# Performance work log

Hardware: AMD Instinct MI355X
Metric: run time of the kernel (lower is better)

The kernel has to match this reference:

```python
import jax, jax.numpy as jnp
import numpy as np

B, T, C = 32, 1536, 768
G, Vg = 2, 160  # num_groups, vars_per_group (num_vars=320)
TEMP = 2.0


def setup_inputs() -> dict:
    key = jax.random.key(0)
    kx, kg, kw, kc = jax.random.split(key, 4)
    x = jax.random.normal(kx, (B, T, C), dtype=jnp.float32)
    # Gumbel(0,1) noise, equivalent to torch's -log(Exp(1).sample())
    gumbel = jax.random.gumbel(kg, (B, T, G, Vg), dtype=jnp.float32)
    W_proj = jax.random.normal(kw, (C, G * Vg), dtype=jnp.float32) * (1.0 / np.sqrt(C))
    b_proj = jnp.zeros((G * Vg,), dtype=jnp.float32)
    codebook = jax.random.normal(kc, (G, Vg, C), dtype=jnp.float32)
    return {"x": x, "gumbel": gumbel, "W_proj": W_proj, "b_proj": b_proj, "codebook": codebook}


def reference(x, gumbel, W_proj, b_proj, codebook):
    b, t, c = x.shape
    g, vg, _ = codebook.shape
    logits = (x @ W_proj + b_proj).reshape(b, t, g, vg)          # (B,T,G,Vg)
    probs = jax.nn.softmax((logits + gumbel) / TEMP, axis=-1)    # (B,T,G,Vg)
    codes = jnp.argmax(probs, axis=-1)                           # (B,T,G)
    # Fused codebook contraction: sum over vars AND groups in one GEMM-like einsum,
    # avoiding the naive (B,T,G,Vg,C) broadcast intermediate.
    quantized = jnp.einsum('btgv,gvc->btc', probs, codebook)     # (B,T,C)
    return quantized, codes, probs
```

## Files before the change

### kernel.cpp

```cpp
#include <hip/hip_runtime.h>
#include <hip/hip_bf16.h>
#include <stdint.h>

#define BT_TOK   49152
#define C_DIM    768
#define NVARS    320
#define VG       160
#define NGROUPS  2

__device__ __forceinline__ unsigned short bf16_rne(float f) {
    union { float f; uint32_t u; } v; v.f = f;
    uint32_t u = v.u + 0x7FFFu + ((v.u >> 16) & 1u);
    return (unsigned short)(u >> 16);
}
__device__ __forceinline__ float bf16_to_f(unsigned short h) {
    union { uint32_t u; float f; } v; v.u = ((uint32_t)h) << 16;
    return v.f;
}

typedef __attribute__((ext_vector_type(8))) short bf16x8;
typedef __attribute__((ext_vector_type(4))) float f32x4;

#define GLOBAL_AS __attribute__((address_space(1)))
#define LDS_AS    __attribute__((address_space(3)))
__device__ __forceinline__ void gl2lds16(const void* g, void* l) {
    __builtin_amdgcn_global_load_lds((const GLOBAL_AS void*)g, (LDS_AS void*)l, 16, 0, 0);
}

__global__ __launch_bounds__(256)
void split_convert(const float* __restrict__ in, unsigned short* __restrict__ hi,
                   unsigned short* __restrict__ lo, int n) {
    int i = (blockIdx.x * 256 + threadIdx.x) * 4;
    if (i >= n) return;
    float4 v = *(const float4*)(in + i);
    ushort4 h, l;
    h.x = bf16_rne(v.x); l.x = bf16_rne(v.x - bf16_to_f(h.x));
    h.y = bf16_rne(v.y); l.y = bf16_rne(v.y - bf16_to_f(h.y));
    h.z = bf16_rne(v.z); l.z = bf16_rne(v.z - bf16_to_f(h.z));
    h.w = bf16_rne(v.w); l.w = bf16_rne(v.w - bf16_to_f(h.w));
    *(ushort4*)(hi + i) = h;
    *(ushort4*)(lo + i) = l;
}

__global__ __launch_bounds__(256)
void transpose_split(const float* __restrict__ in, unsigned short* __restrict__ hi,
                     unsigned short* __restrict__ lo, int K, int N) {
    int k = blockIdx.x * 256 + threadIdx.x;
    int n = blockIdx.y;
    if (k >= K) return;
    float f = in[(size_t)k * N + n];
    unsigned short h = bf16_rne(f);
    hi[(size_t)n * K + k] = h;
    lo[(size_t)n * K + k] = bf16_rne(f - bf16_to_f(h));
}

template<int BM, int BN, int WM, int WN>
__global__ __launch_bounds__(WM*WN*64, (WM*WN+3)/4)
void gemm_split_db(const unsigned short* __restrict__ Ahi, const unsigned short* __restrict__ Alo,
                   const unsigned short* __restrict__ Bthi, const unsigned short* __restrict__ Btlo,
                   const float* __restrict__ bias, float* __restrict__ C,
                   int M, int N, int K)
{
    constexpr int NW = WM * WN;
    constexpr int nIterA = (BM * 4) / 64;
    constexpr int nIterB = (BN * 4) / 64;
    constexpr int ABYTES = BM * 32 * 2;
    constexpr int BBYTES = BN * 32 * 2;
    constexpr int BUFBYTES = 2 * ABYTES + 2 * BBYTES;

    extern __shared__ __align__(16) char smem[];

    const int tid  = threadIdx.x;
    const int lane = tid & 63;
    const int wid  = tid >> 6;
    const int wm   = wid % WM;
    const int wn   = wid / WM;
    const int m0   = blockIdx.y * BM;
    const int n0   = blockIdx.x * BN;

    const int r15 = lane & 15;
    const int q   = lane >> 4;

    f32x4 acc[4][4];
#pragma unroll
    for (int i = 0; i < 4; ++i)
#pragma unroll
        for (int j = 0; j < 4; ++j) {
            f32x4 z = {0.f, 0.f, 0.f, 0.f};
            acc[i][j] = z;
        }

    auto stage = [&](int buf, int k0) {
        char* base = smem + buf * BUFBYTES;
        for (int i = wid; i < nIterA; i += NW) {
            int slot = i * 64 + lane;
            int row  = slot >> 2, cs = slot & 3;
            int c    = cs ^ ((row >> 1) & 3);
            size_t goff = (size_t)(m0 + row) * K + k0 + c * 8;
            gl2lds16(Ahi + goff, base + i * 1024);
            gl2lds16(Alo + goff, base + ABYTES + i * 1024);
        }
        for (int i = wid; i < nIterB; i += NW) {
            int slot = i * 64 + lane;
            int row  = slot >> 2, cs = slot & 3;
            int c    = cs ^ ((row >> 1) & 3);
            size_t goff = (size_t)(n0 + row) * K + k0 + c * 8;
            gl2lds16(Bthi + goff, base + 2 * ABYTES + i * 1024);
            gl2lds16(Btlo + goff, base + 2 * ABYTES + BBYTES + i * 1024);
        }
    };

    const int NT = K / 32;
    stage(0, 0);
    __syncthreads();

    int cur = 0;
    for (int t = 0; t < NT; ++t) {
        if (t + 1 < NT) stage(cur ^ 1, (t + 1) * 32);

        const unsigned short* sAh = (const unsigned short*)(smem + cur * BUFBYTES);
        const unsigned short* sAl = (const unsigned short*)(smem + cur * BUFBYTES + ABYTES);
        const unsigned short* sBh = (const unsigned short*)(smem + cur * BUFBYTES + 2 * ABYTES);
        const unsigned short* sBl = (const unsigned short*)(smem + cur * BUFBYTES + 2 * ABYTES + BBYTES);

        bf16x8 ah[4], al[4], bh[4], bl[4];
#pragma unroll
        for (int mi = 0; mi < 4; ++mi) {
            int row = wm * 64 + mi * 16 + r15;
            int off = row * 32 + ((q ^ ((row >> 1) & 3)) * 8);
            ah[mi] = *(const bf16x8*)&sAh[off];
            al[mi] = *(const bf16x8*)&sAl[off];
        }
#pragma unroll
        for (int ni = 0; ni < 4; ++ni) {
            int row = wn * 64 + ni * 16 + r15;
            int off = row * 32 + ((q ^ ((row >> 1) & 3)) * 8);
            bh[ni] = *(const bf16x8*)&sBh[off];
            bl[ni] = *(const bf16x8*)&sBl[off];
        }

#pragma unroll
        for (int mi = 0; mi < 4; ++mi)
#pragma unroll
            for (int ni = 0; ni < 4; ++ni) {
                acc[mi][ni] = __builtin_amdgcn_mfma_f32_16x16x32_bf16(ah[mi], bh[ni], acc[mi][ni], 0, 0, 0);
                acc[mi][ni] = __builtin_amdgcn_mfma_f32_16x16x32_bf16(ah[mi], bl[ni], acc[mi][ni], 0, 0, 0);
                acc[mi][ni] = __builtin_amdgcn_mfma_f32_16x16x32_bf16(al[mi], bh[ni], acc[mi][ni], 0, 0, 0);
            }

        __syncthreads();
        cur ^= 1;
    }

#pragma unroll
    for (int ni = 0; ni < 4; ++ni) {
        int col = n0 + wn * 64 + ni * 16 + r15;
        float bv = bias ? bias[col] : 0.f;
#pragma unroll
        for (int mi = 0; mi < 4; ++mi) {
            int rbase = m0 + wm * 64 + mi * 16 + q * 4;
#pragma unroll
            for (int rr = 0; rr < 4; ++rr)
                C[(size_t)(rbase + rr) * N + col] = acc[mi][ni][rr] + bv;
        }
    }
}

__global__ __launch_bounds__(256)
void gumbel_softmax_kernel(float* __restrict__ logits_probs,
                           const float* __restrict__ gumbel,
                           float* __restrict__ codes,
                           unsigned short* __restrict__ phi,
                           unsigned short* __restrict__ plo)
{
    const int wid  = (int)((blockIdx.x * (size_t)blockDim.x + threadIdx.x) >> 6);
    const int lane = threadIdx.x & 63;
    if (wid >= BT_TOK * NGROUPS) return;

    float* base        = logits_probs + (size_t)wid * VG;
    const float* gbase = gumbel       + (size_t)wid * VG;

    const float NEG = -3.402823466e+38f;
    float y[3];
    float mx = NEG;
#pragma unroll
    for (int i = 0; i < 3; ++i) {
        int v = lane + i * 64;
        float val = NEG;
        if (v < VG) val = (base[v] + gbase[v]) * 0.5f;
        y[i] = val;
        mx = fmaxf(mx, val);
    }
#pragma unroll
    for (int off = 32; off > 0; off >>= 1)
        mx = fmaxf(mx, __shfl_xor(mx, off, 64));

    float e[3];
    float s = 0.f;
#pragma unroll
    for (int i = 0; i < 3; ++i) {
        int v = lane + i * 64;
        e[i] = (v < VG) ? expf(y[i] - mx) : 0.f;
        s += e[i];
    }
#pragma unroll
    for (int off = 32; off > 0; off >>= 1)
        s += __shfl_xor(s, off, 64);
    const float inv = 1.0f / s;

#pragma unroll
    for (int i = 0; i < 3; ++i) {
        int v = lane + i * 64;
        if (v < VG) {
            float p = e[i] * inv;
            base[v] = p;
            if (phi) {
                unsigned short h = bf16_rne(p);
                phi[(size_t)wid * VG + v] = h;
                plo[(size_t)wid * VG + v] = bf16_rne(p - bf16_to_f(h));
            }
        }
    }

    float bv = y[0];
    int   bi = lane;
#pragma unroll
    for (int i = 1; i < 3; ++i) {
        int v = lane + i * 64;
        if (v < VG && y[i] > bv) { bv = y[i]; bi = v; }
    }
#pragma unroll
    for (int off = 32; off > 0; off >>= 1) {
        float ov = __shfl_xor(bv, off, 64);
        int   oi = __shfl_xor(bi, off, 64);
        if (ov > bv || (ov == bv && oi < bi)) { bv = ov; bi = oi; }
    }
    if (lane == 0) codes[wid] = (float)bi;
}

__global__ __launch_bounds__(256)
void sgemm64(const float* __restrict__ A, const float* __restrict__ B,
             const float* __restrict__ bias, float* __restrict__ C,
             int M, int N, int K)
{
    const int tid = threadIdx.x;
    const int n0  = blockIdx.x * 64;
    const int m0  = blockIdx.y * 64;

    __shared__ float As[16][64 + 4];
    __shared__ float Bs[16][64];

    const int a_row = tid >> 2;
    const int a_k   = (tid & 3) * 4;
    const int b_row = tid >> 4;
    const int b_col = (tid & 15) * 4;
    const int tx = tid & 15;
    const int ty = tid >> 4;

    float acc[4][4] = {};

    for (int k0 = 0; k0 < K; k0 += 16) {
        float4 av = *(const float4*)(A + (size_t)(m0 + a_row) * K + k0 + a_k);
        float4 bv = *(const float4*)(B + (size_t)(k0 + b_row) * N + n0 + b_col);
        __syncthreads();
        As[a_k + 0][a_row] = av.x;
        As[a_k + 1][a_row] = av.y;
        As[a_k + 2][a_row] = av.z;
        As[a_k + 3][a_row] = av.w;
        *(float4*)&Bs[b_row][b_col] = bv;
        __syncthreads();
#pragma unroll
        for (int k = 0; k < 16; ++k) {
            float4 a4 = *(const float4*)&As[k][ty * 4];
            float4 b4 = *(const float4*)&Bs[k][tx * 4];
            const float a[4] = {a4.x, a4.y, a4.z, a4.w};
            const float b[4] = {b4.x, b4.y, b4.z, b4.w};
#pragma unroll
            for (int r = 0; r < 4; ++r)
#pragma unroll
                for (int c = 0; c < 4; ++c)
                    acc[r][c] = fmaf(a[r], b[c], acc[r][c]);
        }
    }

    float4 bs = make_float4(0.f, 0.f, 0.f, 0.f);
    if (bias) bs = *(const float4*)(bias + n0 + tx * 4);
#pragma unroll
    for (int r = 0; r < 4; ++r) {
        float4 o;
        o.x = acc[r][0] + bs.x;
        o.y = acc[r][1] + bs.y;
        o.z = acc[r][2] + bs.z;
        o.w = acc[r][3] + bs.w;
        *(float4*)(C + (size_t)(m0 + ty * 4 + r) * N + n0 + tx * 4) = o;
    }
}

extern "C" void kernel_launch(void* const* d_in, const int* in_sizes, int n_in,
                              void* d_out, int out_size, void* d_ws, size_t ws_size,
                              hipStream_t stream) {
    const float* x        = (const float*)d_in[0];
    const float* gumbel   = (const float*)d_in[1];
    const float* W_proj   = (const float*)d_in[2];
    const float* b_proj   = (const float*)d_in[3];
    const float* codebook = (const float*)d_in[4];

    float* quantized = (float*)d_out;
    float* codes     = quantized + (size_t)BT_TOK * C_DIM;
    float* probs     = codes + (size_t)BT_TOK * NGROUPS;

    const size_t SZ_X  = (size_t)BT_TOK * C_DIM * 2;
    const size_t SZ_P  = (size_t)BT_TOK * NVARS * 2;
    const size_t SZ_W  = (size_t)C_DIM * NVARS * 2;
    const size_t need  = 2 * SZ_X + 2 * SZ_P + 4 * SZ_W;

    constexpr int SH1 = 2 * (2 * (64 * 32 * 2)  + 2 * (320 * 32 * 2));
    constexpr int SH2 = 2 * (2 * (128 * 32 * 2) + 2 * (384 * 32 * 2));

    if (ws_size >= need) {
        static bool s_init = false;
        if (!s_init) {
            hipFuncSetAttribute(reinterpret_cast<const void*>(&gemm_split_db<64, 320, 1, 5>),
                                hipFuncAttributeMaxDynamicSharedMemorySize, SH1);
            hipFuncSetAttribute(reinterpret_cast<const void*>(&gemm_split_db<128, 384, 2, 6>),
                                hipFuncAttributeMaxDynamicSharedMemorySize, SH2);
            s_init = true;
        }

        char* ws = (char*)d_ws;
        unsigned short* xhi  = (unsigned short*)(ws);
        unsigned short* xlo  = (unsigned short*)(ws + SZ_X);
        unsigned short* wthi = (unsigned short*)(ws + 2 * SZ_X);
        unsigned short* wtlo = (unsigned short*)(ws + 2 * SZ_X + SZ_W);
        unsigned short* cthi = (unsigned short*)(ws + 2 * SZ_X + 2 * SZ_W);
        unsigned short* ctlo = (unsigned short*)(ws + 2 * SZ_X + 3 * SZ_W);
        unsigned short* phi  = (unsigned short*)(ws + 2 * SZ_X + 4 * SZ_W);
        unsigned short* plo  = (unsigned short*)(ws + 2 * SZ_X + 4 * SZ_W + SZ_P);

        split_convert<<<(BT_TOK * C_DIM / 4 + 255) / 256, 256, 0, stream>>>(
            x, xhi, xlo, BT_TOK * C_DIM);
        transpose_split<<<dim3((C_DIM + 255) / 256, NVARS), 256, 0, stream>>>(
            W_proj, wthi, wtlo, C_DIM, NVARS);
        transpose_split<<<dim3((NVARS + 255) / 256, C_DIM), 256, 0, stream>>>(
            codebook, cthi, ctlo, NVARS, C_DIM);

        gemm_split_db<64, 320, 1, 5><<<dim3(1, BT_TOK / 64), 320, SH1, stream>>>(
            xhi, xlo, wthi, wtlo, b_proj, probs, BT_TOK, NVARS, C_DIM);

        gumbel_softmax_kernel<<<BT_TOK * NGROUPS / 4, 256, 0, stream>>>(
            probs, gumbel, codes, phi, plo);

        gemm_split_db<128, 384, 2, 6><<<dim3(C_DIM / 384, BT_TOK / 128), 768, SH2, stream>>>(
            phi, plo, cthi, ctlo, nullptr, quantized, BT_TOK, C_DIM, NVARS);
    } else {
        dim3 g1(NVARS / 64, BT_TOK / 64);
        sgemm64<<<g1, 256, 0, stream>>>(x, W_proj, b_proj, probs, BT_TOK, NVARS, C_DIM);
        gumbel_softmax_kernel<<<BT_TOK * NGROUPS / 4, 256, 0, stream>>>(
            probs, gumbel, codes, nullptr, nullptr);
        dim3 g2(C_DIM / 64, BT_TOK / 64);
        sgemm64<<<g2, 256, 0, stream>>>(probs, codebook, nullptr, quantized, BT_TOK, C_DIM, NVARS);
    }
}
```

Before: 578.6 us.

## Fuse bf16 split into GEMM loads and gumbel-softmax into GEMM1 epilogue

Removes the separate split_convert pass over x and the separate gumbel-softmax kernel. GEMM1 now loads fp32 x directly, splits it into hi/lo bf16 in registers, and writes the parts to LDS. Its epilogue stages the logits in LDS and computes softmax, probs and argmax codes in the same kernel. GEMM2 reads fp32 probs and splits them on the fly, so the bf16 workspace copies of x and probs are dropped. This saves large HBM round trips and two launches, at the cost of extra conversion ALU work and register-staged A loads inside the GEMM main loops.

```diff
diff --git a/kernel.cpp b/kernel.cpp
--- a/kernel.cpp
+++ b/kernel.cpp
@@ -25,21 +25,6 @@
 #define LDS_AS    __attribute__((address_space(3)))
 __device__ __forceinline__ void gl2lds16(const void* g, void* l) {
     __builtin_amdgcn_global_load_lds((const GLOBAL_AS void*)g, (LDS_AS void*)l, 16, 0, 0);
-}
-
-__global__ __launch_bounds__(256)
-void split_convert(const float* __restrict__ in, unsigned short* __restrict__ hi,
-                   unsigned short* __restrict__ lo, int n) {
-    int i = (blockIdx.x * 256 + threadIdx.x) * 4;
-    if (i >= n) return;
-    float4 v = *(const float4*)(in + i);
-    ushort4 h, l;
-    h.x = bf16_rne(v.x); l.x = bf16_rne(v.x - bf16_to_f(h.x));
-    h.y = bf16_rne(v.y); l.y = bf16_rne(v.y - bf16_to_f(h.y));
-    h.z = bf16_rne(v.z); l.z = bf16_rne(v.z - bf16_to_f(h.z));
-    h.w = bf16_rne(v.w); l.w = bf16_rne(v.w - bf16_to_f(h.w));
-    *(ushort4*)(hi + i) = h;
-    *(ushort4*)(lo + i) = l;
 }
 
 __global__ __launch_bounds__(256)
@@ -55,14 +40,18 @@
 }
 
 template<int BM, int BN, int WM, int WN>
-__global__ __launch_bounds__(WM*WN*64, (WM*WN+3)/4)
-void gemm_split_db(const unsigned short* __restrict__ Ahi, const unsigned short* __restrict__ Alo,
-                   const unsigned short* __restrict__ Bthi, const unsigned short* __restrict__ Btlo,
-                   const float* __restrict__ bias, float* __restrict__ C,
-                   int M, int N, int K)
+__global__ __launch_bounds__(WM*WN*64, 2)
+void gemm1_softmax_fused(const float* __restrict__ X,
+                         const unsigned short* __restrict__ Bthi,
+                         const unsigned short* __restrict__ Btlo,
+                         const float* __restrict__ bias,
+                         const float* __restrict__ gumbel,
+                         float* __restrict__ probs,
+                         float* __restrict__ codes,
+                         int M, int N, int K)
 {
     constexpr int NW = WM * WN;
-    constexpr int nIterA = (BM * 4) / 64;
+    constexpr int ACH    = BM * 4;
     constexpr int nIterB = (BN * 4) / 64;
     constexpr int ABYTES = BM * 32 * 2;
     constexpr int BBYTES = BN * 32 * 2;
@@ -81,6 +70,12 @@
     const int r15 = lane & 15;
     const int q   = lane >> 4;
 
+    const int arow  = tid >> 2;
+    const int ac    = tid & 3;
+    const int aslot = ac ^ ((arow >> 1) & 3);
+    const float* aptr = X + (size_t)(m0 + arow) * K + ac * 8;
+    const bool adoes = (tid < ACH);
+
     f32x4 acc[4][4];
 #pragma unroll
     for (int i = 0; i < 4; ++i)
@@ -90,33 +85,49 @@
             acc[i][j] = z;
         }
 
-    auto stage = [&](int buf, int k0) {
-        char* base = smem + buf * BUFBYTES;
-        for (int i = wid; i < nIterA; i += NW) {
-            int slot = i * 64 + lane;
-            int row  = slot >> 2, cs = slot & 3;
-            int c    = cs ^ ((row >> 1) & 3);
-            size_t goff = (size_t)(m0 + row) * K + k0 + c * 8;
-            gl2lds16(Ahi + goff, base + i * 1024);
-            gl2lds16(Alo + goff, base + ABYTES + i * 1024);
-        }
+    auto issueB = [&](int buf, int k0) {
+        char* base = smem + buf * BUFBYTES + 2 * ABYTES;
         for (int i = wid; i < nIterB; i += NW) {
             int slot = i * 64 + lane;
             int row  = slot >> 2, cs = slot & 3;
             int c    = cs ^ ((row >> 1) & 3);
             size_t goff = (size_t)(n0 + row) * K + k0 + c * 8;
-            gl2lds16(Bthi + goff, base + 2 * ABYTES + i * 1024);
-            gl2lds16(Btlo + goff, base + 2 * ABYTES + BBYTES + i * 1024);
+            gl2lds16(Bthi + goff, base + i * 1024);
+            gl2lds16(Btlo + goff, base + BBYTES + i * 1024);
         }
     };
 
+    float4 av0, av1;
+    auto loadA = [&](int k0) {
+        if (adoes) {
+            av0 = *(const float4*)(aptr + k0);
+            av1 = *(const float4*)(aptr + k0 + 4);
+        }
+    };
+    auto writeA = [&](int buf) {
+        if (adoes) {
+            char* base = smem + buf * BUFBYTES;
+            union { unsigned short u[8]; bf16x8 v; } h, l;
+            float f[8] = {av0.x, av0.y, av0.z, av0.w, av1.x, av1.y, av1.z, av1.w};
+#pragma unroll
+            for (int j = 0; j < 8; ++j) {
+                h.u[j] = bf16_rne(f[j]);
+                l.u[j] = bf16_rne(f[j] - bf16_to_f(h.u[j]));
+            }
+            *(bf16x8*)(base + arow * 64 + aslot * 16)          = h.v;
+            *(bf16x8*)(base + ABYTES + arow * 64 + aslot * 16) = l.v;
+        }
+    };
+
     const int NT = K / 32;
-    stage(0, 0);
+    loadA(0);
+    issueB(0, 0);
+    writeA(0);
     __syncthreads();
 
     int cur = 0;
     for (int t = 0; t < NT; ++t) {
-        if (t + 1 < NT) stage(cur ^ 1, (t + 1) * 32);
+        if (t + 1 < NT) { loadA((t + 1) * 32); issueB(cur ^ 1, (t + 1) * 32); }
 
         const unsigned short* sAh = (const unsigned short*)(smem + cur * BUFBYTES);
         const unsigned short* sAl = (const unsigned short*)(smem + cur * BUFBYTES + ABYTES);
@@ -148,20 +159,195 @@
                 acc[mi][ni] = __builtin_amdgcn_mfma_f32_16x16x32_bf16(al[mi], bh[ni], acc[mi][ni], 0, 0, 0);
             }
 
+        if (t + 1 < NT) writeA(cur ^ 1);
+
         __syncthreads();
         cur ^= 1;
     }
 
+    float* sL = (float*)smem;
+    constexpr int LSTR = BN + 1;
+#pragma unroll
+    for (int ni = 0; ni < 4; ++ni) {
+        int col = wn * 64 + ni * 16 + r15;
+        float bv = bias[n0 + col];
+#pragma unroll
+        for (int mi = 0; mi < 4; ++mi) {
+            int rbase = wm * 64 + mi * 16 + q * 4;
+#pragma unroll
+            for (int rr = 0; rr < 4; ++rr)
+                sL[(rbase + rr) * LSTR + col] = acc[mi][ni][rr] + bv;
+        }
+    }
+    __syncthreads();
+
+    for (int rg = wid; rg < 2 * BM; rg += NW) {
+        const int r = rg >> 1, g = rg & 1;
+        const float* gsrc = gumbel + (size_t)(m0 + r) * NVARS + g * VG;
+        const float* lrow = sL + r * LSTR + g * VG;
+        const bool  has2 = (lane < VG - 128);
+
+        float y0 = (lrow[lane]       + gsrc[lane])       * 0.5f;
+        float y1 = (lrow[lane + 64]  + gsrc[lane + 64])  * 0.5f;
+        float y2 = has2 ? (lrow[lane + 128] + gsrc[lane + 128]) * 0.5f
+                        : -3.402823466e+38f;
+
+        float mx = fmaxf(fmaxf(y0, y1), y2);
+#pragma unroll
+        for (int off = 32; off > 0; off >>= 1)
+            mx = fmaxf(mx, __shfl_xor(mx, off, 64));
+
+        float e0 = expf(y0 - mx);
+        float e1 = expf(y1 - mx);
+        float e2 = has2 ? expf(y2 - mx) : 0.f;
+        float s  = e0 + e1 + e2;
+#pragma unroll
+        for (int off = 32; off > 0; off >>= 1)
+            s += __shfl_xor(s, off, 64);
+        const float inv = 1.0f / s;
+
+        float* prow = probs + (size_t)(m0 + r) * NVARS + g * VG;
+        prow[lane]      = e0 * inv;
+        prow[lane + 64] = e1 * inv;
+        if (has2) prow[lane + 128] = e2 * inv;
+
+        float bvv = y0; int bii = lane;
+        if (y1 > bvv) { bvv = y1; bii = lane + 64; }
+        if (has2 && y2 > bvv) { bvv = y2; bii = lane + 128; }
+#pragma unroll
+        for (int off = 32; off > 0; off >>= 1) {
+            float ov = __shfl_xor(bvv, off, 64);
+            int   oi = __shfl_xor(bii, off, 64);
+            if (ov > bvv || (ov == bvv && oi < bii)) { bvv = ov; bii = oi; }
+        }
+        if (lane == 0) codes[(size_t)(m0 + r) * NGROUPS + g] = (float)bii;
+    }
+}
+
+template<int BM, int BN, int WM, int WN>
+__global__ __launch_bounds__(WM*WN*64, (WM*WN+3)/4)
+void gemm2_fused(const float* __restrict__ P,
+                 const unsigned short* __restrict__ Bthi,
+                 const unsigned short* __restrict__ Btlo,
+                 float* __restrict__ C,
+                 int M, int N, int K)
+{
+    constexpr int NW = WM * WN;
+    constexpr int ACH    = BM * 4;
+    constexpr int nIterB = (BN * 4) / 64;
+    constexpr int ABYTES = BM * 32 * 2;
+    constexpr int BBYTES = BN * 32 * 2;
+    constexpr int BUFBYTES = 2 * ABYTES + 2 * BBYTES;
+
+    extern __shared__ __align__(16) char smem[];
+
+    const int tid  = threadIdx.x;
+    const int lane = tid & 63;
+    const int wid  = tid >> 6;
+    const int wm   = wid % WM;
+    const int wn   = wid / WM;
+    const int m0   = blockIdx.y * BM;
+    const int n0   = blockIdx.x * BN;
+
+    const int r15 = lane & 15;
+    const int q   = lane >> 4;
+
+    const int arow  = tid >> 2;
+    const int ac    = tid & 3;
+    const int aslot = ac ^ ((arow >> 1) & 3);
+    const float* aptr = P + (size_t)(m0 + arow) * K + ac * 8;
+    const bool adoes = (tid < ACH);
+
+    f32x4 acc[4][4];
+#pragma unroll
+    for (int i = 0; i < 4; ++i)
+#pragma unroll
+        for (int j = 0; j < 4; ++j) {
+            f32x4 z = {0.f, 0.f, 0.f, 0.f};
+            acc[i][j] = z;
+        }
+
+    auto issueB = [&](int buf, int k0) {
+        char* base = smem + buf * BUFBYTES + 2 * ABYTES;
+        for (int i = wid; i < nIterB; i += NW) {
+            int slot = i * 64 + lane;
+            int row  = slot >> 2, cs = slot & 3;
+            int c    = cs ^ ((row >> 1) & 3);
+            size_t goff = (size_t)(n0 + row) * K + k0 + c * 8;
+            gl2lds16(Bthi + goff, base + i * 1024);
+            gl2lds16(Btlo + goff, base + BBYTES + i * 1024);
+        }
+    };
+
+    auto stageA = [&](int buf, int k0) {
+        if (adoes) {
+            float4 av0 = *(const float4*)(aptr + k0);
+            float4 av1 = *(const float4*)(aptr + k0 + 4);
+            char* base = smem + buf * BUFBYTES;
+            union { unsigned short u[8]; bf16x8 v; } h, l;
+            float f[8] = {av0.x, av0.y, av0.z, av0.w, av1.x, av1.y, av1.z, av1.w};
+#pragma unroll
+            for (int j = 0; j < 8; ++j) {
+                h.u[j] = bf16_rne(f[j]);
+                l.u[j] = bf16_rne(f[j] - bf16_to_f(h.u[j]));
+            }
+            *(bf16x8*)(base + arow * 64 + aslot * 16)          = h.v;
+            *(bf16x8*)(base + ABYTES + arow * 64 + aslot * 16) = l.v;
+        }
+    };
+
+    const int NT = K / 32;
+    issueB(0, 0);
+    stageA(0, 0);
+    __syncthreads();
+
+    int cur = 0;
+    for (int t = 0; t < NT; ++t) {
+        if (t + 1 < NT) { issueB(cur ^ 1, (t + 1) * 32); stageA(cur ^ 1, (t + 1) * 32); }
+
+        const unsigned short* sAh = (const unsigned short*)(smem + cur * BUFBYTES);
+        const unsigned short* sAl = (const unsigned short*)(smem + cur * BUFBYTES + ABYTES);
+        const unsigned short* sBh = (const unsigned short*)(smem + cur * BUFBYTES + 2 * ABYTES);
+        const unsigned short* sBl = (const unsigned short*)(smem + cur * BUFBYTES + 2 * ABYTES + BBYTES);
+
+        bf16x8 ah[4], al[4], bh[4], bl[4];
+#pragma unroll
+        for (int mi = 0; mi < 4; ++mi) {
+            int row = wm * 64 + mi * 16 + r15;
+            int off = row * 32 + ((q ^ ((row >> 1) & 3)) * 8);
+            ah[mi] = *(const bf16x8*)&sAh[off];
+            al[mi] = *(const bf16x8*)&sAl[off];
+        }
+#pragma unroll
+        for (int ni = 0; ni < 4; ++ni) {
+            int row = wn * 64 + ni * 16 + r15;
+            int off = row * 32 + ((q ^ ((row >> 1) & 3)) * 8);
+            bh[ni] = *(const bf16x8*)&sBh[off];
+            bl[ni] = *(const bf16x8*)&sBl[off];
+        }
+
+#pragma unroll
+        for (int mi = 0; mi < 4; ++mi)
+#pragma unroll
+            for (int ni = 0; ni < 4; ++ni) {
+                acc[mi][ni] = __builtin_amdgcn_mfma_f32_16x16x32_bf16(ah[mi], bh[ni], acc[mi][ni], 0, 0, 0);
+                acc[mi][ni] = __builtin_amdgcn_mfma_f32_16x16x32_bf16(ah[mi], bl[ni], acc[mi][ni], 0, 0, 0);
+                acc[mi][ni] = __builtin_amdgcn_mfma_f32_16x16x32_bf16(al[mi], bh[ni], acc[mi][ni], 0, 0, 0);
+            }
+
+        __syncthreads();
+        cur ^= 1;
+    }
+
 #pragma unroll
     for (int ni = 0; ni < 4; ++ni) {
         int col = n0 + wn * 64 + ni * 16 + r15;
-        float bv = bias ? bias[col] : 0.f;
 #pragma unroll
         for (int mi = 0; mi < 4; ++mi) {
             int rbase = m0 + wm * 64 + mi * 16 + q * 4;
 #pragma unroll
             for (int rr = 0; rr < 4; ++rr)
-                C[(size_t)(rbase + rr) * N + col] = acc[mi][ni][rr] + bv;
+                C[(size_t)(rbase + rr) * N + col] = acc[mi][ni][rr];
         }
     }
 }
@@ -309,10 +495,8 @@
     float* codes     = quantized + (size_t)BT_TOK * C_DIM;
     float* probs     = codes + (size_t)BT_TOK * NGROUPS;
 
-    const size_t SZ_X  = (size_t)BT_TOK * C_DIM * 2;
-    const size_t SZ_P  = (size_t)BT_TOK * NVARS * 2;
     const size_t SZ_W  = (size_t)C_DIM * NVARS * 2;
-    const size_t need  = 2 * SZ_X + 2 * SZ_P + 4 * SZ_W;
+    const size_t need  = 4 * SZ_W;
 
     constexpr int SH1 = 2 * (2 * (64 * 32 * 2)  + 2 * (320 * 32 * 2));
     constexpr int SH2 = 2 * (2 * (128 * 32 * 2) + 2 * (384 * 32 * 2));
@@ -320,38 +504,29 @@
     if (ws_size >= need) {
         static bool s_init = false;
         if (!s_init) {
-            hipFuncSetAttribute(reinterpret_cast<const void*>(&gemm_split_db<64, 320, 1, 5>),
+            hipFuncSetAttribute(reinterpret_cast<const void*>(&gemm1_softmax_fused<64, 320, 1, 5>),
                                 hipFuncAttributeMaxDynamicSharedMemorySize, SH1);
-            hipFuncSetAttribute(reinterpret_cast<const void*>(&gemm_split_db<128, 384, 2, 6>),
+            hipFuncSetAttribute(reinterpret_cast<const void*>(&gemm2_fused<128, 384, 2, 6>),
                                 hipFuncAttributeMaxDynamicSharedMemorySize, SH2);
             s_init = true;
         }
 
         char* ws = (char*)d_ws;
-        unsigned short* xhi  = (unsigned short*)(ws);
-        unsigned short* xlo  = (unsigned short*)(ws + SZ_X);
-        unsigned short* wthi = (unsigned short*)(ws + 2 * SZ_X);
-        unsigned short* wtlo = (unsigned short*)(ws + 2 * SZ_X + SZ_W);
-        unsigned short* cthi = (unsigned short*)(ws + 2 * SZ_X + 2 * SZ_W);
-        unsigned short* ctlo = (unsigned short*)(ws + 2 * SZ_X + 3 * SZ_W);
-        unsigned short* phi  = (unsigned short*)(ws + 2 * SZ_X + 4 * SZ_W);
-        unsigned short* plo  = (unsigned short*)(ws + 2 * SZ_X + 4 * SZ_W + SZ_P);
-
-        split_convert<<<(BT_TOK * C_DIM / 4 + 255) / 256, 256, 0, stream>>>(
-            x, xhi, xlo, BT_TOK * C_DIM);
+        unsigned short* wthi = (unsigned short*)(ws);
+        unsigned short* wtlo = (unsigned short*)(ws + SZ_W);
+        unsigned short* cthi = (unsigned short*)(ws + 2 * SZ_W);
+        unsigned short* ctlo = (unsigned short*)(ws + 3 * SZ_W);
+
         transpose_split<<<dim3((C_DIM + 255) / 256, NVARS), 256, 0, stream>>>(
             W_proj, wthi, wtlo, C_DIM, NVARS);
         transpose_split<<<dim3((NVARS + 255) / 256, C_DIM), 256, 0, stream>>>(
             codebook, cthi, ctlo, NVARS, C_DIM);
 
-        gemm_split_db<64, 320, 1, 5><<<dim3(1, BT_TOK / 64), 320, SH1, stream>>>(
-            xhi, xlo, wthi, wtlo, b_proj, probs, BT_TOK, NVARS, C_DIM);
-
-        gumbel_softmax_kernel<<<BT_TOK * NGROUPS / 4, 256, 0, stream>>>(
-            probs, gumbel, codes, phi, plo);
-
-        gemm_split_db<128, 384, 2, 6><<<dim3(C_DIM / 384, BT_TOK / 128), 768, SH2, stream>>>(
-            phi, plo, cthi, ctlo, nullptr, quantized, BT_TOK, C_DIM, NVARS);
+        gemm1_softmax_fused<64, 320, 1, 5><<<dim3(1, BT_TOK / 64), 320, SH1, stream>>>(
+            x, wthi, wtlo, b_proj, gumbel, probs, codes, BT_TOK, NVARS, C_DIM);
+
+        gemm2_fused<128, 384, 2, 6><<<dim3(C_DIM / 384, BT_TOK / 128), 768, SH2, stream>>>(
+            probs, cthi, ctlo, quantized, BT_TOK, C_DIM, NVARS);
     } else {
         dim3 g1(NVARS / 64, BT_TOK / 64);
         sgemm64<<<g1, 256, 0, stream>>>(x, W_proj, b_proj, probs, BT_TOK, NVARS, C_DIM);
```

After: 615.8 us. 1.06x slower.
